# Performance work log

Measured on AMD Instinct MI355X. Metric: run time of the kernel, lower is better.

## Reference

```python
import jax, jax.numpy as jnp
import numpy as np

ATTN_HEADS = 4
NEG_INF = float(np.finfo(np.float32).min)


def setup_inputs() -> dict:
    key = jax.random.key(0)
    ks = jax.random.split(key, 7)
    B, N, K, Cin, Cout = 4, 4096, 32, 128, 128
    h_X = jax.random.normal(ks[0], (B, N, Cout), dtype=jnp.float32)
    h_E = jax.random.normal(ks[1], (B, N, K, Cin), dtype=jnp.float32)
    mask_attn = jax.random.randint(ks[2], (B, N, K), 0, 2, dtype=jnp.int32)
    # torch Linear weights are [out_features, in_features]
    W_Q = jax.random.normal(ks[3], (Cout, Cout), dtype=jnp.float32) / np.sqrt(Cout)
    W_K = jax.random.normal(ks[4], (Cout, Cin), dtype=jnp.float32) / np.sqrt(Cin)
    W_V = jax.random.normal(ks[5], (Cout, Cin), dtype=jnp.float32) / np.sqrt(Cin)
    W_O = jax.random.normal(ks[6], (Cout, 3 * Cout), dtype=jnp.float32) / np.sqrt(3 * Cout)
    return {"h_X": h_X, "h_E": h_E, "mask_attn": mask_attn,
            "W_Q": W_Q, "W_K": W_K, "W_V": W_V, "W_O": W_O}


def reference(h_X, h_E, mask_attn, W_Q, W_K, W_V, W_O):
    B, N, K, _ = h_E.shape
    C = W_Q.shape[0]
    H = ATTN_HEADS
    d = C // H

    h_q = (h_X @ W_Q.T).reshape(B, N, H, d)          # [B,N,H,d]
    h_k = (h_E @ W_K.T).reshape(B, N, K, H, d)       # [B,N,K,H,d]
    h_v = (h_E @ W_V.T).reshape(B, N, K, H, d)       # [B,N,K,H,d]

    # per-node, per-head scores over K neighbors
    scores = jnp.einsum('bnhd,bnkhd->bnhk', h_q, h_k) / np.sqrt(d)

    mask = (mask_attn[:, :, None, :] > 0)            # [B,N,1,K] -> broadcast over heads
    logits = jnp.where(mask, scores, NEG_INF)
    attn = jax.nn.softmax(logits, axis=-1) * mask.astype(scores.dtype)  # [B,N,H,K]

    attn_sum = attn.sum(axis=-1, keepdims=True) + 1e-8                  # [B,N,H,1]
    hv_t = jnp.swapaxes(h_v, 2, 3)                                      # [B,N,H,K,d]
    weighted_v = attn[..., None] * hv_t                                 # [B,N,H,K,d]
    weighted_sum = weighted_v.sum(axis=3)                               # [B,N,H,d]
    aggr_mean = (weighted_sum / attn_sum).reshape(B, N, C)
    aggr_sum = weighted_sum.reshape(B, N, C)
    aggr_max = weighted_v.max(axis=3).reshape(B, N, C)

    aggr_cat = jnp.concatenate([aggr_mean, aggr_sum, aggr_max], axis=-1)  # [B,N,3C]
    return aggr_cat @ W_O.T                                               # [B,N,C]
```

## Files before the change

kernel.cpp:

```cpp
#include <hip/hip_runtime.h>
#include <hip/hip_bf16.h>
#include <stdint.h>


typedef __attribute__((ext_vector_type(8))) short short8;
typedef __attribute__((ext_vector_type(4))) float f32x4;

#define NPB   16
#define CDIM  128
#define KN    32
#define ESTR  136
#define CATS  392
#define NEGI  -3.0e38f

__device__ __forceinline__ float bf2f(short s) {
    union { unsigned int u; float f; } v;
    v.u = ((unsigned int)(unsigned short)s) << 16;
    return v.f;
}
__device__ __forceinline__ short f2bf(float f) {
    union { float ff; unsigned int u; } v; v.ff = f;
    unsigned int u = v.u;
    u += 0x7FFFu + ((u >> 16) & 1u);
    return (short)(u >> 16);
}

__device__ __forceinline__ short8 cvt8(const f32x4& a, const f32x4& b) {
    union { __hip_bfloat162 h; unsigned int u; } c0, c1, c2, c3;
    c0.h = __float22bfloat162_rn(float2{a[0], a[1]});
    c1.h = __float22bfloat162_rn(float2{a[2], a[3]});
    c2.h = __float22bfloat162_rn(float2{b[0], b[1]});
    c3.h = __float22bfloat162_rn(float2{b[2], b[3]});
    short8 r;
    r[0] = (short)(c0.u & 0xffff); r[1] = (short)(c0.u >> 16);
    r[2] = (short)(c1.u & 0xffff); r[3] = (short)(c1.u >> 16);
    r[4] = (short)(c2.u & 0xffff); r[5] = (short)(c2.u >> 16);
    r[6] = (short)(c3.u & 0xffff); r[7] = (short)(c3.u >> 16);
    return r;
}

template<bool FP32>
__device__ __forceinline__ short8 load8bf(const void* p, size_t idx) {
    if constexpr (FP32) {
        const float* fp = (const float*)p + idx;
        f32x4 a = *(const f32x4*)fp;
        f32x4 b = *(const f32x4*)(fp + 4);
        return cvt8(a, b);
    } else {
        return *(const short8*)((const short*)p + idx);
    }
}

template<bool FP32>
__device__ __forceinline__ short loadbf1(const void* p, size_t idx) {
    if constexpr (FP32) return f2bf(((const float*)p)[idx]);
    else return ((const short*)p)[idx];
}

__device__ __forceinline__ bool detect_fp32(const short* wp) {
    const int lane = threadIdx.x & 63;
    int cnt = 0;
    #pragma unroll
    for (int i = 0; i < 8; ++i) {
        const float v = bf2f(wp[lane + i * 64]);
        if (!(fabsf(v) < 8.0f)) cnt++;
    }
    #pragma unroll
    for (int d = 1; d < 64; d <<= 1) cnt += __shfl_xor(cnt, d);
    return cnt > 16;
}

struct alignas(16) Smem {
    short sEb[2][32 * ESTR];
    short sT[64 * ESTR];
    union {
        short sQ[16 * ESTR];
        short sCat[16 * CATS];
    } u;
    int   sMask[NPB * KN];
};

template<bool FP32>
__device__ __forceinline__ void issueN(const void* hE, size_t base, int tid,
                                       f32x4 (&pF)[2][2], short8 (&pB)[2]) {
    if constexpr (FP32) {
        #pragma unroll
        for (int it = 0; it < 2; ++it) {
            const float* p = (const float*)hE + base + (size_t)(it * 256 + tid) * 8;
            pF[it][0] = *(const f32x4*)p;
            pF[it][1] = *(const f32x4*)(p + 4);
        }
    } else {
        #pragma unroll
        for (int it = 0; it < 2; ++it)
            pB[it] = *(const short8*)((const short*)hE + base + (size_t)(it * 256 + tid) * 8);
    }
    __builtin_amdgcn_sched_barrier(0);
}

template<bool FP32>
__device__ __forceinline__ void writeN(short* dst, int tid,
                                       const f32x4 (&pF)[2][2], const short8 (&pB)[2]) {
    #pragma unroll
    for (int it = 0; it < 2; ++it) {
        const int chunk = it * 256 + tid, row = chunk >> 4, cc = chunk & 15;
        short8 v;
        if constexpr (FP32) v = cvt8(pF[it][0], pF[it][1]);
        else                v = pB[it];
        *(short8*)&dst[row * ESTR + cc * 8] = v;
    }
}

template<bool FP32>
__device__ __forceinline__ void na_body(Smem& sm,
    const void* __restrict__ hX, const void* __restrict__ hE,
    const int* __restrict__ mask, const void* __restrict__ WQ,
    const void* __restrict__ WK, const void* __restrict__ WV,
    const void* __restrict__ WO, void* __restrict__ out)
{
    const int tid  = threadIdx.x;
    const int lane = tid & 63;
    const int w    = tid >> 6;
    const int quad = lane >> 4;
    const int l15  = lane & 15;
    const int nb   = blockIdx.x * NPB;
    const size_t ebase = (size_t)nb * (KN * CDIM);

    f32x4 pF[2][2]; short8 pB[2];
    issueN<FP32>(hE, ebase, tid, pF, pB);

    *(int2*)&sm.sMask[tid * 2] = *(const int2*)&mask[(size_t)nb * KN + tid * 2];

    short8 ax[4];
    #pragma unroll
    for (int kk = 0; kk < 4; ++kk)
        ax[kk] = load8bf<FP32>(hX, (size_t)(nb + l15) * CDIM + kk * 32 + quad * 8);
    short8 bq[2][4];
    #pragma unroll
    for (int t2 = 0; t2 < 2; ++t2)
        #pragma unroll
        for (int kk = 0; kk < 4; ++kk)
            bq[t2][kk] = load8bf<FP32>(WQ, (size_t)(w * 32 + t2 * 16 + l15) * CDIM + kk * 32 + quad * 8);
    {
        f32x4 o0 = {0.f,0.f,0.f,0.f}, o1 = {0.f,0.f,0.f,0.f};
        #pragma unroll
        for (int kk = 0; kk < 4; ++kk) {
            o0 = __builtin_amdgcn_mfma_f32_16x16x32_bf16(ax[kk], bq[0][kk], o0, 0, 0, 0);
            o1 = __builtin_amdgcn_mfma_f32_16x16x32_bf16(ax[kk], bq[1][kk], o1, 0, 0, 0);
        }
        #pragma unroll
        for (int r = 0; r < 4; ++r) {
            const int n = quad * 4 + r;
            sm.u.sQ[n * ESTR + w * 32 + l15]      = f2bf(o0[r]);
            sm.u.sQ[n * ESTR + w * 32 + 16 + l15] = f2bf(o1[r]);
        }
    }
    __syncthreads();

    short8 bk[2][4];
    #pragma unroll
    for (int t2 = 0; t2 < 2; ++t2)
        #pragma unroll
        for (int kk = 0; kk < 4; ++kk) {
            const int j = w * 32 + t2 * 16 + l15;
            short8 b;
            #pragma unroll
            for (int jj = 0; jj < 8; ++jj)
                b[jj] = loadbf1<FP32>(WK, (size_t)(kk * 32 + quad * 8 + jj) * CDIM + j);
            bk[t2][kk] = b;
        }
    {
        const float scale = 0.17677669529663687f;
        const short8 zz = {0,0,0,0,0,0,0,0};
        #pragma unroll
        for (int m = 0; m < 4; ++m) {
            const int n_g = m * 4 + (l15 >> 2), h_ = l15 & 3;
            const short8 qv = *(const short8*)&sm.u.sQ[n_g * ESTR + h_ * 32 + quad * 8];
            f32x4 c0 = {0.f,0.f,0.f,0.f}, c1 = {0.f,0.f,0.f,0.f};
            #pragma unroll
            for (int kk = 0; kk < 4; ++kk) {
                const short8 af = (kk == h_) ? qv : zz;
                c0 = __builtin_amdgcn_mfma_f32_16x16x32_bf16(af, bk[0][kk], c0, 0, 0, 0);
                c1 = __builtin_amdgcn_mfma_f32_16x16x32_bf16(af, bk[1][kk], c1, 0, 0, 0);
            }
            #pragma unroll
            for (int r = 0; r < 4; ++r) {
                const int row = m * 16 + quad * 4 + r;
                sm.sT[row * ESTR + w * 32 + l15]      = f2bf(c0[r] * scale);
                sm.sT[row * ESTR + w * 32 + 16 + l15] = f2bf(c1[r] * scale);
            }
        }
    }

    short8 bv[2][4];
    #pragma unroll
    for (int ct2 = 0; ct2 < 2; ++ct2)
        #pragma unroll
        for (int kk = 0; kk < 4; ++kk)
            bv[ct2][kk] = load8bf<FP32>(WV, (size_t)((2 * w + ct2) * 16 + l15) * CDIM + kk * 32 + quad * 8);

    writeN<FP32>(sm.sEb[0], tid, pF, pB);
    issueN<FP32>(hE, ebase + 1 * (KN * CDIM), tid, pF, pB);
    __syncthreads();

    #pragma unroll 1
    for (int i = 0; i < NPB; ++i) {
        const short* bufp = sm.sEb[i & 1];

        short8 a0[4], a1[4], bs[4];
        #pragma unroll
        for (int kk = 0; kk < 4; ++kk) {
            bs[kk] = *(const short8*)&sm.sT[(i * 4 + (l15 & 3)) * ESTR + kk * 32 + quad * 8];
            a0[kk] = *(const short8*)&bufp[l15 * ESTR + kk * 32 + quad * 8];
            a1[kk] = *(const short8*)&bufp[(16 + l15) * ESTR + kk * 32 + quad * 8];
        }

        f32x4 s0 = {0.f,0.f,0.f,0.f}, s1 = {0.f,0.f,0.f,0.f};
        #pragma unroll
        for (int kk = 0; kk < 4; ++kk) {
            s0 = __builtin_amdgcn_mfma_f32_16x16x32_bf16(a0[kk], bs[kk], s0, 0, 0, 0);
            s1 = __builtin_amdgcn_mfma_f32_16x16x32_bf16(a1[kk], bs[kk], s1, 0, 0, 0);
        }

        float x[8], ainv;
        {
            const int* mp = &sm.sMask[i * KN];
            int mk[8];
            #pragma unroll
            for (int j = 0; j < 4; ++j) {
                x[j] = s0[j];     mk[j]     = mp[quad * 4 + j];
                x[4 + j] = s1[j]; mk[4 + j] = mp[16 + quad * 4 + j];
            }
            float m = NEGI;
            #pragma unroll
            for (int j = 0; j < 8; ++j) m = fmaxf(m, (mk[j] > 0) ? x[j] : NEGI);
            m = fmaxf(m, __shfl_xor(m, 16));
            m = fmaxf(m, __shfl_xor(m, 32));
            float dsum = 0.f;
            #pragma unroll
            for (int j = 0; j < 8; ++j) {
                const float e = __expf(fminf(x[j] - m, 0.f)) * ((mk[j] > 0) ? 1.f : 0.f);
                x[j] = e; dsum += e;
            }
            dsum += __shfl_xor(dsum, 16);
            dsum += __shfl_xor(dsum, 32);
            const float inv = (dsum > 0.f) ? (1.f / dsum) : 0.f;
            #pragma unroll
            for (int j = 0; j < 8; ++j) x[j] *= inv;
            ainv = 1.0f / (((dsum > 0.f) ? 1.0f : 0.0f) + 1e-8f);
        }

        if (i < NPB - 1) {
            writeN<FP32>(sm.sEb[(i + 1) & 1], tid, pF, pB);
            if (i < NPB - 2)
                issueN<FP32>(hE, ebase + (size_t)(i + 2) * (KN * CDIM), tid, pF, pB);
        }

        {
            const int src = (quad << 4) | w;
            float aA[4], aB[4];
            #pragma unroll
            for (int r = 0; r < 4; ++r) {
                aA[r] = __shfl(x[r], src);
                aB[r] = __shfl(x[4 + r], src);
            }
            const float ainvw = __shfl(ainv, src);
            #pragma unroll
            for (int ct2 = 0; ct2 < 2; ++ct2) {
                f32x4 av0 = {0.f,0.f,0.f,0.f}, av1 = {0.f,0.f,0.f,0.f};
                #pragma unroll
                for (int kk = 0; kk < 4; ++kk) {
                    av0 = __builtin_amdgcn_mfma_f32_16x16x32_bf16(a0[kk], bv[ct2][kk], av0, 0, 0, 0);
                    av1 = __builtin_amdgcn_mfma_f32_16x16x32_bf16(a1[kk], bv[ct2][kk], av1, 0, 0, 0);
                }
                float sum = 0.f, mx = NEGI;
                #pragma unroll
                for (int r = 0; r < 4; ++r) {
                    const float p0 = aA[r] * av0[r];
                    const float p1 = aB[r] * av1[r];
                    sum += p0 + p1;
                    mx = fmaxf(mx, fmaxf(p0, p1));
                }
                sum += __shfl_xor(sum, 16);
                sum += __shfl_xor(sum, 32);
                mx = fmaxf(mx, __shfl_xor(mx, 16));
                mx = fmaxf(mx, __shfl_xor(mx, 32));
                if (quad == 0) {
                    const int c = (2 * w + ct2) * 16 + l15;
                    sm.u.sCat[i * CATS + c]       = f2bf(sum * ainvw);
                    sm.u.sCat[i * CATS + 128 + c] = f2bf(sum);
                    sm.u.sCat[i * CATS + 256 + c] = f2bf(mx);
                }
            }
        }
        __syncthreads();
    }

    {
        f32x4 o0 = {0.f,0.f,0.f,0.f}, o1 = {0.f,0.f,0.f,0.f};
        #pragma unroll
        for (int kk = 0; kk < 12; ++kk) {
            const short8 a  = *(const short8*)&sm.u.sCat[l15 * CATS + kk * 32 + quad * 8];
            const short8 b0 = load8bf<FP32>(WO, (size_t)(w * 32 + l15) * 384 + kk * 32 + quad * 8);
            const short8 b1 = load8bf<FP32>(WO, (size_t)(w * 32 + 16 + l15) * 384 + kk * 32 + quad * 8);
            o0 = __builtin_amdgcn_mfma_f32_16x16x32_bf16(a, b0, o0, 0, 0, 0);
            o1 = __builtin_amdgcn_mfma_f32_16x16x32_bf16(a, b1, o1, 0, 0, 0);
        }
        #pragma unroll
        for (int r = 0; r < 4; ++r) {
            const int node = quad * 4 + r;
            const size_t base = (size_t)(nb + node) * CDIM + w * 32;
            if constexpr (FP32) {
                ((float*)out)[base + l15]      = o0[r];
                ((float*)out)[base + 16 + l15] = o1[r];
            } else {
                ((short*)out)[base + l15]      = f2bf(o0[r]);
                ((short*)out)[base + 16 + l15] = f2bf(o1[r]);
            }
        }
    }
}

__global__ __launch_bounds__(256, 3)
void na_fused(const void* __restrict__ hX, const void* __restrict__ hE,
              const int* __restrict__ mask, const void* __restrict__ WQ,
              const void* __restrict__ WK, const void* __restrict__ WV,
              const void* __restrict__ WO, void* __restrict__ out)
{
    __shared__ Smem sm;
    if (detect_fp32((const short*)WQ)) na_body<true >(sm, hX, hE, mask, WQ, WK, WV, WO, out);
    else                               na_body<false>(sm, hX, hE, mask, WQ, WK, WV, WO, out);
}

extern "C" void kernel_launch(void* const* d_in, const int* in_sizes, int n_in,
                              void* d_out, int out_size, void* d_ws, size_t ws_size,
                              hipStream_t stream) {
    (void)in_sizes; (void)n_in; (void)ws_size; (void)out_size; (void)d_ws;
    const void* hX   = d_in[0];
    const void* hE   = d_in[1];
    const int*  mask = (const int*)d_in[2];
    const void* WQ   = d_in[3];
    const void* WK   = d_in[4];
    const void* WV   = d_in[5];
    const void* WO   = d_in[6];

    na_fused<<<dim3(1024), dim3(256), 0, stream>>>(hX, hE, mask, WQ, WK, WV, WO, d_out);
}
```

Measured before the change: 398.2 us.

## Assign whole nodes per wave with register-prefetched edges, dropping shared edge buffers

Each wave now processes its own 8 nodes end to end. Edge features are loaded straight into MFMA register fragments with a one-node-ahead register prefetch, which replaces the block-wide double-buffered LDS staging and the per-node __syncthreads. Block size grows to 32 nodes (512 blocks), the mask is packed into bits via ballot, and each wave holds all V-weight fragments (bv[8][4]). This raises register pressure, so launch bounds drop to 2 blocks per CU, and 512 blocks may leave some CUs underfilled.

```diff
diff --git a/kernel.cpp b/kernel.cpp
--- a/kernel.cpp
+++ b/kernel.cpp
@@ -6,7 +6,8 @@
 typedef __attribute__((ext_vector_type(8))) short short8;
 typedef __attribute__((ext_vector_type(4))) float f32x4;
 
-#define NPB   16
+#define NPB   32
+#define WPN   8
 #define CDIM  128
 #define KN    32
 #define ESTR  136
@@ -71,43 +72,131 @@
 }
 
 struct alignas(16) Smem {
-    short sEb[2][32 * ESTR];
-    short sT[64 * ESTR];
+    short sT[128 * ESTR];
     union {
-        short sQ[16 * ESTR];
-        short sCat[16 * CATS];
+        short sQ[32 * ESTR];
+        short sCat[32 * CATS];
     } u;
-    int   sMask[NPB * KN];
+    int      sMask[NPB * KN];
+    unsigned sMaskBits[NPB];
 };
 
 template<bool FP32>
-__device__ __forceinline__ void issueN(const void* hE, size_t base, int tid,
-                                       f32x4 (&pF)[2][2], short8 (&pB)[2]) {
-    if constexpr (FP32) {
-        #pragma unroll
-        for (int it = 0; it < 2; ++it) {
-            const float* p = (const float*)hE + base + (size_t)(it * 256 + tid) * 8;
-            pF[it][0] = *(const f32x4*)p;
-            pF[it][1] = *(const f32x4*)(p + 4);
-        }
-    } else {
-        #pragma unroll
-        for (int it = 0; it < 2; ++it)
-            pB[it] = *(const short8*)((const short*)hE + base + (size_t)(it * 256 + tid) * 8);
+__device__ __forceinline__ void issueE(const void* hE, size_t gnode,
+                                       int quad, int l15,
+                                       f32x4 (&rF)[8][2], short8 (&rB)[8]) {
+    const size_t eb = gnode * (size_t)(KN * CDIM);
+    #pragma unroll
+    for (int t = 0; t < 8; ++t) {
+        const int row = (t & 4) ? (16 + l15) : l15;
+        const size_t idx = eb + (size_t)row * CDIM + (t & 3) * 32 + quad * 8;
+        if constexpr (FP32) {
+            const float* p = (const float*)hE + idx;
+            rF[t][0] = *(const f32x4*)p;
+            rF[t][1] = *(const f32x4*)(p + 4);
+        } else {
+            rB[t] = *(const short8*)((const short*)hE + idx);
+        }
     }
     __builtin_amdgcn_sched_barrier(0);
 }
 
 template<bool FP32>
-__device__ __forceinline__ void writeN(short* dst, int tid,
-                                       const f32x4 (&pF)[2][2], const short8 (&pB)[2]) {
-    #pragma unroll
-    for (int it = 0; it < 2; ++it) {
-        const int chunk = it * 256 + tid, row = chunk >> 4, cc = chunk & 15;
-        short8 v;
-        if constexpr (FP32) v = cvt8(pF[it][0], pF[it][1]);
-        else                v = pB[it];
-        *(short8*)&dst[row * ESTR + cc * 8] = v;
+__device__ __forceinline__ void cvtE(const f32x4 (&rF)[8][2], const short8 (&rB)[8],
+                                     short8 (&aE)[8]) {
+    #pragma unroll
+    for (int t = 0; t < 8; ++t) {
+        if constexpr (FP32) aE[t] = cvt8(rF[t][0], rF[t][1]);
+        else                aE[t] = rB[t];
+    }
+}
+
+template<bool FP32>
+__device__ __forceinline__ void procNode(Smem& sm, int nl, const short8 (&aE)[8],
+                                         const short8 (&bv)[8][4],
+                                         int quad, int l15)
+{
+    short8 tq[4];
+    #pragma unroll
+    for (int kk = 0; kk < 4; ++kk)
+        tq[kk] = *(const short8*)&sm.sT[(nl * 4 + (l15 & 3)) * ESTR + kk * 32 + quad * 8];
+
+    const unsigned mb = sm.sMaskBits[nl];
+    const int mk0 = (mb >> l15) & 1;
+    const int mk1 = (mb >> (16 + l15)) & 1;
+
+    f32x4 s0 = {0.f,0.f,0.f,0.f}, s1 = {0.f,0.f,0.f,0.f};
+    #pragma unroll
+    for (int kk = 0; kk < 4; ++kk) {
+        s0 = __builtin_amdgcn_mfma_f32_16x16x32_bf16(tq[kk], aE[kk],     s0, 0, 0, 0);
+        s1 = __builtin_amdgcn_mfma_f32_16x16x32_bf16(tq[kk], aE[4 + kk], s1, 0, 0, 0);
+    }
+
+    float x0[4], x1[4], ainv[4];
+    {
+        float m[4], ds[4];
+        #pragma unroll
+        for (int r = 0; r < 4; ++r) {
+            const float a = mk0 ? s0[r] : NEGI;
+            const float b = mk1 ? s1[r] : NEGI;
+            m[r] = fmaxf(a, b);
+        }
+        #pragma unroll
+        for (int d = 1; d < 16; d <<= 1)
+            #pragma unroll
+            for (int r = 0; r < 4; ++r) m[r] = fmaxf(m[r], __shfl_xor(m[r], d));
+        #pragma unroll
+        for (int r = 0; r < 4; ++r) {
+            x0[r] = __expf(fminf(s0[r] - m[r], 0.f)) * (mk0 ? 1.f : 0.f);
+            x1[r] = __expf(fminf(s1[r] - m[r], 0.f)) * (mk1 ? 1.f : 0.f);
+            ds[r] = x0[r] + x1[r];
+        }
+        #pragma unroll
+        for (int d = 1; d < 16; d <<= 1)
+            #pragma unroll
+            for (int r = 0; r < 4; ++r) ds[r] += __shfl_xor(ds[r], d);
+        #pragma unroll
+        for (int r = 0; r < 4; ++r) {
+            const float inv = (ds[r] > 0.f) ? (1.f / ds[r]) : 0.f;
+            x0[r] *= inv; x1[r] *= inv;
+            ainv[r] = 1.0f / (((ds[r] > 0.f) ? 1.0f : 0.0f) + 1e-8f);
+        }
+    }
+
+    const size_t ng = (size_t)nl * CATS;
+    #pragma unroll
+    for (int ct = 0; ct < 8; ++ct) {
+        const int h = ct >> 1;
+        float aA[4], aB[4];
+        #pragma unroll
+        for (int r = 0; r < 4; ++r) {
+            aA[r] = __shfl(x0[h], quad * 4 + r);
+            aB[r] = __shfl(x1[h], quad * 4 + r);
+        }
+        f32x4 av0 = {0.f,0.f,0.f,0.f}, av1 = {0.f,0.f,0.f,0.f};
+        #pragma unroll
+        for (int kk = 0; kk < 4; ++kk) {
+            av0 = __builtin_amdgcn_mfma_f32_16x16x32_bf16(aE[kk],     bv[ct][kk], av0, 0, 0, 0);
+            av1 = __builtin_amdgcn_mfma_f32_16x16x32_bf16(aE[4 + kk], bv[ct][kk], av1, 0, 0, 0);
+        }
+        float sum = 0.f, mx = NEGI;
+        #pragma unroll
+        for (int r = 0; r < 4; ++r) {
+            const float p0 = aA[r] * av0[r];
+            const float p1 = aB[r] * av1[r];
+            sum += p0 + p1;
+            mx = fmaxf(mx, fmaxf(p0, p1));
+        }
+        sum += __shfl_xor(sum, 16);
+        sum += __shfl_xor(sum, 32);
+        mx = fmaxf(mx, __shfl_xor(mx, 16));
+        mx = fmaxf(mx, __shfl_xor(mx, 32));
+        if (quad == 0) {
+            const int c = ct * 16 + l15;
+            sm.u.sCat[ng + c]       = f2bf(sum * ainv[h]);
+            sm.u.sCat[ng + 128 + c] = f2bf(sum);
+            sm.u.sCat[ng + 256 + c] = f2bf(mx);
+        }
     }
 }
 
@@ -124,56 +213,66 @@
     const int quad = lane >> 4;
     const int l15  = lane & 15;
     const int nb   = blockIdx.x * NPB;
-    const size_t ebase = (size_t)nb * (KN * CDIM);
-
-    f32x4 pF[2][2]; short8 pB[2];
-    issueN<FP32>(hE, ebase, tid, pF, pB);
-
-    *(int2*)&sm.sMask[tid * 2] = *(const int2*)&mask[(size_t)nb * KN + tid * 2];
-
-    short8 ax[4];
-    #pragma unroll
-    for (int kk = 0; kk < 4; ++kk)
-        ax[kk] = load8bf<FP32>(hX, (size_t)(nb + l15) * CDIM + kk * 32 + quad * 8);
-    short8 bq[2][4];
-    #pragma unroll
-    for (int t2 = 0; t2 < 2; ++t2)
-        #pragma unroll
-        for (int kk = 0; kk < 4; ++kk)
-            bq[t2][kk] = load8bf<FP32>(WQ, (size_t)(w * 32 + t2 * 16 + l15) * CDIM + kk * 32 + quad * 8);
+
+    f32x4 rF[8][2]; short8 rB[8];
+    issueE<FP32>(hE, (size_t)(nb + w * WPN), quad, l15, rF, rB);
+
+    *(int4*)&sm.sMask[tid * 4] = *(const int4*)&mask[(size_t)nb * KN + tid * 4];
+
     {
-        f32x4 o0 = {0.f,0.f,0.f,0.f}, o1 = {0.f,0.f,0.f,0.f};
-        #pragma unroll
-        for (int kk = 0; kk < 4; ++kk) {
-            o0 = __builtin_amdgcn_mfma_f32_16x16x32_bf16(ax[kk], bq[0][kk], o0, 0, 0, 0);
-            o1 = __builtin_amdgcn_mfma_f32_16x16x32_bf16(ax[kk], bq[1][kk], o1, 0, 0, 0);
-        }
-        #pragma unroll
-        for (int r = 0; r < 4; ++r) {
-            const int n = quad * 4 + r;
-            sm.u.sQ[n * ESTR + w * 32 + l15]      = f2bf(o0[r]);
-            sm.u.sQ[n * ESTR + w * 32 + 16 + l15] = f2bf(o1[r]);
+        short8 bq[2][4];
+        #pragma unroll
+        for (int t2 = 0; t2 < 2; ++t2)
+            #pragma unroll
+            for (int kk = 0; kk < 4; ++kk)
+                bq[t2][kk] = load8bf<FP32>(WQ, (size_t)(w * 32 + t2 * 16 + l15) * CDIM + kk * 32 + quad * 8);
+        #pragma unroll
+        for (int mt = 0; mt < 2; ++mt) {
+            short8 ax[4];
+            #pragma unroll
+            for (int kk = 0; kk < 4; ++kk)
+                ax[kk] = load8bf<FP32>(hX, (size_t)(nb + mt * 16 + l15) * CDIM + kk * 32 + quad * 8);
+            f32x4 o0 = {0.f,0.f,0.f,0.f}, o1 = {0.f,0.f,0.f,0.f};
+            #pragma unroll
+            for (int kk = 0; kk < 4; ++kk) {
+                o0 = __builtin_amdgcn_mfma_f32_16x16x32_bf16(ax[kk], bq[0][kk], o0, 0, 0, 0);
+                o1 = __builtin_amdgcn_mfma_f32_16x16x32_bf16(ax[kk], bq[1][kk], o1, 0, 0, 0);
+            }
+            #pragma unroll
+            for (int r = 0; r < 4; ++r) {
+                const int n = mt * 16 + quad * 4 + r;
+                sm.u.sQ[n * ESTR + w * 32 + l15]      = f2bf(o0[r]);
+                sm.u.sQ[n * ESTR + w * 32 + 16 + l15] = f2bf(o1[r]);
+            }
         }
     }
     __syncthreads();
 
-    short8 bk[2][4];
-    #pragma unroll
-    for (int t2 = 0; t2 < 2; ++t2)
-        #pragma unroll
-        for (int kk = 0; kk < 4; ++kk) {
-            const int j = w * 32 + t2 * 16 + l15;
-            short8 b;
-            #pragma unroll
-            for (int jj = 0; jj < 8; ++jj)
-                b[jj] = loadbf1<FP32>(WK, (size_t)(kk * 32 + quad * 8 + jj) * CDIM + j);
-            bk[t2][kk] = b;
-        }
+    #pragma unroll
+    for (int t = 0; t < WPN; ++t) {
+        const int n = w * WPN + t;
+        const bool bit = (lane < 32) && (sm.sMask[n * KN + (lane & 31)] > 0);
+        const unsigned long long bal = __ballot(bit);
+        if (lane == 0) sm.sMaskBits[n] = (unsigned)bal;
+    }
+
     {
+        short8 bk[2][4];
+        #pragma unroll
+        for (int t2 = 0; t2 < 2; ++t2)
+            #pragma unroll
+            for (int kk = 0; kk < 4; ++kk) {
+                const int j = w * 32 + t2 * 16 + l15;
+                short8 b;
+                #pragma unroll
+                for (int jj = 0; jj < 8; ++jj)
+                    b[jj] = loadbf1<FP32>(WK, (size_t)(kk * 32 + quad * 8 + jj) * CDIM + j);
+                bk[t2][kk] = b;
+            }
         const float scale = 0.17677669529663687f;
         const short8 zz = {0,0,0,0,0,0,0,0};
         #pragma unroll
-        for (int m = 0; m < 4; ++m) {
+        for (int m = 0; m < 8; ++m) {
             const int n_g = m * 4 + (l15 >> 2), h_ = l15 & 3;
             const short8 qv = *(const short8*)&sm.u.sQ[n_g * ESTR + h_ * 32 + quad * 8];
             f32x4 c0 = {0.f,0.f,0.f,0.f}, c1 = {0.f,0.f,0.f,0.f};
@@ -192,115 +291,32 @@
         }
     }
 
-    short8 bv[2][4];
-    #pragma unroll
-    for (int ct2 = 0; ct2 < 2; ++ct2)
+    short8 bv[8][4];
+    #pragma unroll
+    for (int ct = 0; ct < 8; ++ct)
         #pragma unroll
         for (int kk = 0; kk < 4; ++kk)
-            bv[ct2][kk] = load8bf<FP32>(WV, (size_t)((2 * w + ct2) * 16 + l15) * CDIM + kk * 32 + quad * 8);
-
-    writeN<FP32>(sm.sEb[0], tid, pF, pB);
-    issueN<FP32>(hE, ebase + 1 * (KN * CDIM), tid, pF, pB);
+            bv[ct][kk] = load8bf<FP32>(WV, (size_t)(ct * 16 + l15) * CDIM + kk * 32 + quad * 8);
+
     __syncthreads();
 
+    short8 aE[8];
     #pragma unroll 1
-    for (int i = 0; i < NPB; ++i) {
-        const short* bufp = sm.sEb[i & 1];
-
-        short8 a0[4], a1[4], bs[4];
-        #pragma unroll
-        for (int kk = 0; kk < 4; ++kk) {
-            bs[kk] = *(const short8*)&sm.sT[(i * 4 + (l15 & 3)) * ESTR + kk * 32 + quad * 8];
-            a0[kk] = *(const short8*)&bufp[l15 * ESTR + kk * 32 + quad * 8];
-            a1[kk] = *(const short8*)&bufp[(16 + l15) * ESTR + kk * 32 + quad * 8];
-        }
-
-        f32x4 s0 = {0.f,0.f,0.f,0.f}, s1 = {0.f,0.f,0.f,0.f};
-        #pragma unroll
-        for (int kk = 0; kk < 4; ++kk) {
-            s0 = __builtin_amdgcn_mfma_f32_16x16x32_bf16(a0[kk], bs[kk], s0, 0, 0, 0);
-            s1 = __builtin_amdgcn_mfma_f32_16x16x32_bf16(a1[kk], bs[kk], s1, 0, 0, 0);
-        }
-
-        float x[8], ainv;
-        {
-            const int* mp = &sm.sMask[i * KN];
-            int mk[8];
-            #pragma unroll
-            for (int j = 0; j < 4; ++j) {
-                x[j] = s0[j];     mk[j]     = mp[quad * 4 + j];
-                x[4 + j] = s1[j]; mk[4 + j] = mp[16 + quad * 4 + j];
-            }
-            float m = NEGI;
-            #pragma unroll
-            for (int j = 0; j < 8; ++j) m = fmaxf(m, (mk[j] > 0) ? x[j] : NEGI);
-            m = fmaxf(m, __shfl_xor(m, 16));
-            m = fmaxf(m, __shfl_xor(m, 32));
-            float dsum = 0.f;
-            #pragma unroll
-            for (int j = 0; j < 8; ++j) {
-                const float e = __expf(fminf(x[j] - m, 0.f)) * ((mk[j] > 0) ? 1.f : 0.f);
-                x[j] = e; dsum += e;
-            }
-            dsum += __shfl_xor(dsum, 16);
-            dsum += __shfl_xor(dsum, 32);
-            const float inv = (dsum > 0.f) ? (1.f / dsum) : 0.f;
-            #pragma unroll
-            for (int j = 0; j < 8; ++j) x[j] *= inv;
-            ainv = 1.0f / (((dsum > 0.f) ? 1.0f : 0.0f) + 1e-8f);
-        }
-
-        if (i < NPB - 1) {
-            writeN<FP32>(sm.sEb[(i + 1) & 1], tid, pF, pB);
-            if (i < NPB - 2)
-                issueN<FP32>(hE, ebase + (size_t)(i + 2) * (KN * CDIM), tid, pF, pB);
-        }
-
-        {
-            const int src = (quad << 4) | w;
-            float aA[4], aB[4];
-            #pragma unroll
-            for (int r = 0; r < 4; ++r) {
-                aA[r] = __shfl(x[r], src);
-                aB[r] = __shfl(x[4 + r], src);
-            }
-            const float ainvw = __shfl(ainv, src);
-            #pragma unroll
-            for (int ct2 = 0; ct2 < 2; ++ct2) {
-                f32x4 av0 = {0.f,0.f,0.f,0.f}, av1 = {0.f,0.f,0.f,0.f};
-                #pragma unroll
-                for (int kk = 0; kk < 4; ++kk) {
-                    av0 = __builtin_amdgcn_mfma_f32_16x16x32_bf16(a0[kk], bv[ct2][kk], av0, 0, 0, 0);
-                    av1 = __builtin_amdgcn_mfma_f32_16x16x32_bf16(a1[kk], bv[ct2][kk], av1, 0, 0, 0);
-                }
-                float sum = 0.f, mx = NEGI;
-                #pragma unroll
-                for (int r = 0; r < 4; ++r) {
-                    const float p0 = aA[r] * av0[r];
-                    const float p1 = aB[r] * av1[r];
-                    sum += p0 + p1;
-                    mx = fmaxf(mx, fmaxf(p0, p1));
-                }
-                sum += __shfl_xor(sum, 16);
-                sum += __shfl_xor(sum, 32);
-                mx = fmaxf(mx, __shfl_xor(mx, 16));
-                mx = fmaxf(mx, __shfl_xor(mx, 32));
-                if (quad == 0) {
-                    const int c = (2 * w + ct2) * 16 + l15;
-                    sm.u.sCat[i * CATS + c]       = f2bf(sum * ainvw);
-                    sm.u.sCat[i * CATS + 128 + c] = f2bf(sum);
-                    sm.u.sCat[i * CATS + 256 + c] = f2bf(mx);
-                }
-            }
-        }
-        __syncthreads();
-    }
-
-    {
+    for (int i = 0; i < WPN; ++i) {
+        const int nl = w * WPN + i;
+        cvtE<FP32>(rF, rB, aE);
+        if (i + 1 < WPN)
+            issueE<FP32>(hE, (size_t)(nb + nl + 1), quad, l15, rF, rB);
+        procNode<FP32>(sm, nl, aE, bv, quad, l15);
+    }
+    __syncthreads();
+
+    #pragma unroll
+    for (int mt = 0; mt < 2; ++mt) {
         f32x4 o0 = {0.f,0.f,0.f,0.f}, o1 = {0.f,0.f,0.f,0.f};
         #pragma unroll
         for (int kk = 0; kk < 12; ++kk) {
-            const short8 a  = *(const short8*)&sm.u.sCat[l15 * CATS + kk * 32 + quad * 8];
+            const short8 a  = *(const short8*)&sm.u.sCat[(mt * 16 + l15) * CATS + kk * 32 + quad * 8];
             const short8 b0 = load8bf<FP32>(WO, (size_t)(w * 32 + l15) * 384 + kk * 32 + quad * 8);
             const short8 b1 = load8bf<FP32>(WO, (size_t)(w * 32 + 16 + l15) * 384 + kk * 32 + quad * 8);
             o0 = __builtin_amdgcn_mfma_f32_16x16x32_bf16(a, b0, o0, 0, 0, 0);
@@ -308,7 +324,7 @@
         }
         #pragma unroll
         for (int r = 0; r < 4; ++r) {
-            const int node = quad * 4 + r;
+            const int node = mt * 16 + quad * 4 + r;
             const size_t base = (size_t)(nb + node) * CDIM + w * 32;
             if constexpr (FP32) {
                 ((float*)out)[base + l15]      = o0[r];
@@ -321,7 +337,7 @@
     }
 }
 
-__global__ __launch_bounds__(256, 3)
+__global__ __launch_bounds__(256, 2)
 void na_fused(const void* __restrict__ hX, const void* __restrict__ hE,
               const int* __restrict__ mask, const void* __restrict__ WQ,
               const void* __restrict__ WK, const void* __restrict__ WV,
@@ -344,5 +360,5 @@
     const void* WV   = d_in[5];
     const void* WO   = d_in[6];
 
-    na_fused<<<dim3(1024), dim3(256), 0, stream>>>(hX, hE, mask, WQ, WK, WV, WO, d_out);
-}
+    na_fused<<<dim3(512), dim3(256), 0, stream>>>(hX, hE, mask, WQ, WK, WV, WO, d_out);
+}
```

After: 431.2 us. +8.3%, slower.
